# Kernel tuning notes

Measured on AMD Instinct MI355X. Metric: run time of the kernel, lower is better.

## Reference

```python
import math
import jax, jax.numpy as jnp
import numpy as np

N = 1600; C_IN = 16; HID = 64; OUT = 64; D_K = 8; N_HEADS = 8
CUTS = 8; NUM_RBF = 8; RBF_PROJ = 4; RADIUS = 6.0; ALPHA = 3.0

def leaky(x):
    return jnp.where(x >= 0, x, 0.2 * x)

def group_norm(x, gamma, beta, groups=4, eps=1e-5):
    # x: [N, C]; torch GroupNorm applied on [1, C, N]: stats over (C/groups, N) per group
    n, c = x.shape
    xg = x.T.reshape(groups, -1)
    mu = jnp.mean(xg, axis=1, keepdims=True)
    var = jnp.mean((xg - mu) ** 2, axis=1, keepdims=True)
    xn = ((xg - mu) * jax.lax.rsqrt(var + eps)).reshape(c, n).T
    return xn * gamma + beta

def setup_inputs():
    key = jax.random.key(0)
    ks = jax.random.split(key, 32)
    def rn(k, shape, s=0.1):
        return (jax.random.normal(k, shape) * s).astype(jnp.float32)
    return {
        "points": jax.random.normal(ks[0], (N, 3), jnp.float32),
        "nuv": jax.random.normal(ks[1], (N, 3, 3), jnp.float32),
        "features": jax.random.normal(ks[2], (N, C_IN), jnp.float32),
        "w_in1": rn(ks[3], (HID, C_IN)), "b_in1": rn(ks[4], (HID,)),
        "w_in2": rn(ks[5], (HID, HID)), "b_in2": rn(ks[6], (HID,)),
        "g_in": 1.0 + rn(ks[7], (HID,)), "be_in": rn(ks[8], (HID,)),
        "wq": rn(ks[9], (HID, HID)), "bq": rn(ks[10], (HID,)),
        "wk": rn(ks[11], (HID, HID)), "bk": rn(ks[12], (HID,)),
        "wv": rn(ks[13], (HID, HID)), "bv": rn(ks[14], (HID,)),
        "conv_w1": rn(ks[15], (CUTS, 4 + RBF_PROJ), 0.5),
        "conv_b1": jnp.abs(rn(ks[16], (CUTS,), 0.5)),
        "conv_w2": rn(ks[17], (HID, CUTS), 0.3), "conv_b2": rn(ks[18], (HID,), 0.3),
        "rbf_log_sigma": jnp.log(jnp.asarray(0.6 * 2.0 / (NUM_RBF - 1), jnp.float32)),
        "rbf_a": rn(ks[19], (RBF_PROJ, NUM_RBF), 0.3), "rbf_b": rn(ks[20], (RBF_PROJ,), 0.1),
        "rbf_centers": jnp.linspace(0.0, 2.0, NUM_RBF, dtype=jnp.float32),
        "w_o1": rn(ks[21], (OUT, HID)), "b_o1": rn(ks[22], (OUT,)),
        "w_o2": rn(ks[23], (OUT, OUT)), "b_o2": rn(ks[24], (OUT,)),
        "g_out": 1.0 + rn(ks[25], (OUT,)), "be_out": rn(ks[26], (OUT,)),
        "w_res": rn(ks[27], (OUT, C_IN)), "b_res": rn(ks[28], (OUT,)),
    }

def reference(points, nuv, features, w_in1, b_in1, w_in2, b_in2, g_in, be_in,
              wq, bq, wk, bk, wv, bv, conv_w1, conv_b1, conv_w2, conv_b2,
              rbf_log_sigma, rbf_a, rbf_b, rbf_centers,
              w_o1, b_o1, w_o2, b_o2, g_out, be_out, w_res, b_res):
    # point-wise MLP + GroupNorm
    h = leaky(features @ w_in1.T + b_in1)
    h = leaky(h @ w_in2.T + b_in2)
    h = group_norm(h, g_in, be_in)
    Q = h @ wq.T + bq
    K = h @ wk.T + bk
    V = h @ wv.T + bv
    pts = points / (math.sqrt(2.0) * RADIUS)
    diff = pts[None, :, :] - pts[:, None, :]            # [N, N, 3] = x_j - x_i
    n_i = nuv[:, 0, :]
    n_j = jax.lax.stop_gradient(n_i)                    # j-side normals are detached in the original
    ndot = jnp.einsum("ia,ja->ij", n_i, n_j)            # <n_i, n_j>
    d2 = jnp.sum(diff ** 2, axis=-1) * (2.0 - ndot) ** 2  # pseudo-geodesic squared distance
    W = (1.0 + d2 / ALPHA) ** (-ALPHA)                  # geodesic window weight
    d2_safe = jnp.where(d2 > 0, d2, 1.0)
    base_d = jnp.where(d2 > 0, jnp.sqrt(d2_safe), 0.0)  # safe sqrt (finite grad at 0)
    sigma = jnp.maximum(jnp.exp(rbf_log_sigma), 1e-6)
    R = jnp.exp(-((base_d[:, :, None] - rbf_centers) ** 2) / (2.0 * sigma ** 2))  # [N,N,NUM_RBF]
    R_proj = R @ rbf_a.T + rbf_b                        # [N, N, RBF_PROJ]
    X_loc = jnp.einsum("iab,ijb->ija", nuv, diff)       # local tangent-frame coords [N,N,3]
    X = jnp.concatenate([X_loc, ndot[:, :, None], R_proj], axis=-1)  # [N, N, 4+RBF_PROJ]
    F1 = jax.nn.relu(X @ conv_w1.T + conv_b1)           # shared conv layer-1 [N, N, CUTS]
    scale = 1.0 / math.sqrt(D_K)
    heads = []
    for h_id in range(N_HEADS):
        s = slice(h_id * D_K, (h_id + 1) * D_K)
        Fh = jax.nn.relu(F1 @ conv_w2[s].T + conv_b2[s])      # per-head conv weights [N, N, D_K]
        S = (Q[:, s] @ K[:, s].T) * scale                     # attention logits [N, N]
        P = jax.nn.softmax(S, axis=1) * W                     # softmax over j, fused with window
        heads.append(jnp.einsum("ij,ijc,jc->ic", P, Fh, V[:, s]))
    agg = jnp.concatenate(heads, axis=1)                      # [N, HID]
    o = leaky(agg @ w_o1.T + b_o1)
    o = leaky(o @ w_o2.T + b_o2)
    o = group_norm(o, g_out, be_out)
    return o + features @ w_res.T + b_res
```

## Files before the change

kernel.cpp:

```cpp
#include <hip/hip_runtime.h>

typedef __fp16 h2 __attribute__((ext_vector_type(2)));
typedef unsigned int u32;

#define NPTS 1600
#define NCHUNK 10
#define CHUNKJ 160
#define TILE 32
#define QS (0.35355339059327373f*1.4426950408889634f)
#define PSCALE 0.11785113019775793f
#define LOG2E 1.4426950408889634f

__device__ __forceinline__ float leaky(float x){ return x >= 0.f ? x : 0.2f*x; }
__device__ __forceinline__ float d4(float4 a, float4 b){ return a.x*b.x + a.y*b.y + a.z*b.z + a.w*b.w; }
__device__ __forceinline__ u32 pkn(float a, float b){ h2 v; v[0]=(__fp16)a; v[1]=(__fp16)b; return __builtin_bit_cast(u32,v); }
__device__ __forceinline__ h2 u2h(u32 u){ return __builtin_bit_cast(h2,u); }
__device__ __forceinline__ float dot2(h2 a, h2 b, float c){ return __builtin_amdgcn_fdot2(a,b,c,false); }
__device__ __forceinline__ u32 rfl(u32 x){ return (u32)__builtin_amdgcn_readfirstlane((int)x); }

__global__ __launch_bounds__(256) void k_in(
    const float* __restrict__ feat, const float* __restrict__ w1, const float* __restrict__ b1,
    const float* __restrict__ w2, const float* __restrict__ b2,
    const float* __restrict__ conv_w1, const float* __restrict__ conv_b1,
    const float* __restrict__ conv_w2,
    const float* __restrict__ rbf_a, const float* __restrict__ rbf_b,
    const float* __restrict__ rbf_ls, const float* __restrict__ rbf_c,
    float* __restrict__ h2out, float* __restrict__ bstat1, float* __restrict__ wpk)
{
  __shared__ float sh[4][64];
  __shared__ float sred[4][8];
  int t = threadIdx.x, w = t>>6, c = t&63;
  int i = blockIdx.x*4 + w;

  if (blockIdx.x == 0) {
    u32* wp = (u32*)wpk;
    {
      int row = t>>2, q = t&3;
      wp[32 + row*4 + q] = pkn(conv_w2[row*8+2*q], conv_w2[row*8+2*q+1]);
    }
    if (t < 32) {
      int cc = t>>2, kq = t&3;
      float a0=0.f, a1=0.f;
      #pragma unroll
      for (int p=0;p<4;p++){ a0 += conv_w1[cc*8+4+p]*rbf_a[p*8+2*kq]; a1 += conv_w1[cc*8+4+p]*rbf_a[p*8+2*kq+1]; }
      wp[cc*4+kq] = pkn(a0,a1);
    } else if (t < 40) {
      int cc = t-32; float s = conv_b1[cc];
      #pragma unroll
      for (int p=0;p<4;p++) s += conv_w1[cc*8+4+p]*rbf_b[p];
      wpk[288+cc] = s;
    } else if (t == 40) {
      float sig = fmaxf(expf(rbf_ls[0]), 1e-6f);
      float m = -LOG2E/(2.f*sig*sig);
      float c0 = rbf_c[0];
      float dl = rbf_c[1] - rbf_c[0];
      wpk[296] = c0;
      wpk[297] = m;
      wpk[298] = -2.f*m*dl;
      wpk[299] = m*dl*dl;
    }
  }

  const float4* f4 = (const float4*)(feat + i*16);
  float4 f0=f4[0], f1v=f4[1], f2v=f4[2], f3v=f4[3];
  const float4* w1r = (const float4*)(w1 + c*16);
  float h1 = b1[c] + d4(f0,w1r[0]) + d4(f1v,w1r[1]) + d4(f2v,w1r[2]) + d4(f3v,w1r[3]);
  h1 = leaky(h1);
  sh[w][c] = h1;
  __syncthreads();
  float hh = b2[c];
  #pragma unroll
  for (int k4=0;k4<16;k4++){
    float4 hv = *(const float4*)&sh[w][k4*4];
    hh += d4(hv, *(const float4*)&w2[c*64 + k4*4]);
  }
  hh = leaky(hh);
  h2out[i*64+c] = hh;

  float s = hh, qq = hh*hh;
  s += __shfl_xor(s,1);  qq += __shfl_xor(qq,1);
  s += __shfl_xor(s,2);  qq += __shfl_xor(qq,2);
  s += __shfl_xor(s,4);  qq += __shfl_xor(qq,4);
  s += __shfl_xor(s,8);  qq += __shfl_xor(qq,8);
  if ((c&15)==0){ int g=c>>4; sred[w][g]=s; sred[w][4+g]=qq; }
  __syncthreads();
  if (t<8) bstat1[blockIdx.x*8+t] = sred[0][t]+sred[1][t]+sred[2][t]+sred[3][t];
}

__global__ __launch_bounds__(256) void k_qkv(
  const float* __restrict__ h2b, const float* __restrict__ bstat1,
  const float* __restrict__ g_in, const float* __restrict__ be_in,
  const float* __restrict__ wq, const float* __restrict__ bq,
  const float* __restrict__ wk, const float* __restrict__ bk,
  const float* __restrict__ wv, const float* __restrict__ bv,
  float* __restrict__ Q, float* __restrict__ K, float* __restrict__ V)
{
  __shared__ float sh[4][64];
  __shared__ float sp[64];
  __shared__ float sst[8];
  int t=threadIdx.x, w=t>>6, c=t&63;
  int i = blockIdx.x*4 + w;
  if (t<64){ int g=t&7; float s=0.f;
    for (int m=t>>3; m<400; m+=8) s += bstat1[m*8+g];
    sp[t]=s; }
  __syncthreads();
  if (t<8){ float s=0.f;
    #pragma unroll
    for (int q=0;q<8;q++) s += sp[q*8+t];
    sst[t]=s; }
  __syncthreads();
  int g = c>>4;
  const float inv = 1.f/25600.f;
  float mu = sst[g]*inv;
  float var = sst[4+g]*inv - mu*mu;
  float rs = rsqrtf(var + 1e-5f);
  float hn = (h2b[i*64+c]-mu)*rs*g_in[c] + be_in[c];
  sh[w][c] = hn;
  __syncthreads();
  float q=bq[c], k=bk[c], v=bv[c];
  #pragma unroll
  for (int k4=0;k4<16;k4++){
    float4 hv = *(const float4*)&sh[w][k4*4];
    q += d4(hv, *(const float4*)&wq[c*64+k4*4]);
    k += d4(hv, *(const float4*)&wk[c*64+k4*4]);
    v += d4(hv, *(const float4*)&wv[c*64+k4*4]);
  }
  Q[i*64+c] = q*QS;
  K[i*64+c] = k;
  V[i*64+c] = v;
}

__global__ __launch_bounds__(256,4) void k_pair(
  const float* __restrict__ Qm, const float* __restrict__ Km, const float* __restrict__ Vm,
  const float* __restrict__ pts, const float* __restrict__ nuv,
  const float* __restrict__ w1, const float* __restrict__ wpk,
  const float* __restrict__ b2g, float* __restrict__ part)
{
  __shared__ __align__(16) float SM[4928];
  float* sQ  = SM;
  float* sK  = SM + 1088;
  u32*   sVp = (u32*)(SM + 3264);
  u32*   sWX = (u32*)(SM + 4352);
  float* sPt = SM + 4672;
  float* sNj = SM + 4800;
  float* sRed = SM;

  int t = threadIdx.x;
  int r = t & 15, jl = t >> 4;
  int bx = blockIdx.x;
  int rb = bx % 100, jc = bx / 100;
  int I0 = rb*16, J0 = jc*CHUNKJ;
  int i = I0 + r;

  { int row = t>>4, col = (t&15)<<2;
    *(float4*)&sQ[row*68+col] = *(const float4*)&Qm[(I0+row)*64 + col]; }
  if (t < 128) {
    int r2 = t>>3, cc = t&7, ib = (I0+r2)*9;
    float a0=w1[cc*8], a1=w1[cc*8+1], a2=w1[cc*8+2];
    float x = a0*nuv[ib+0] + a1*nuv[ib+3] + a2*nuv[ib+6];
    float y = a0*nuv[ib+1] + a1*nuv[ib+4] + a2*nuv[ib+7];
    float z = a0*nuv[ib+2] + a1*nuv[ib+5] + a2*nuv[ib+8];
    sWX[r2*20+cc*2+0] = pkn(x,y);
    sWX[r2*20+cc*2+1] = pkn(z, w1[cc*8+3]);
  }
  __syncthreads();
  u32 wxp[16];
  #pragma unroll
  for (int q2=0;q2<4;q2++) *(uint4*)&wxp[q2*4] = *(const uint4*)&sWX[r*20+q2*4];

  const u32* wp = (const u32*)wpk;
  h2 wr[8][4];
  #pragma unroll
  for (int cc=0;cc<8;cc++)
    #pragma unroll
    for (int q2=0;q2<4;q2++) wr[cc][q2] = u2h(rfl(wp[cc*4+q2]));
  const u32* w2p = wp + 32;
  const float* b1p = wpk + 288;
  float c0  = wpk[296];
  float mco = wpk[297];
  float C2  = wpk[298];
  float A1  = wpk[299];

  float pix = pts[i*3+0]*PSCALE, piy = pts[i*3+1]*PSCALE, piz = pts[i*3+2]*PSCALE;
  float nix = nuv[i*9+0], niy = nuv[i*9+1], niz = nuv[i*9+2];

  float acc[64];
  #pragma unroll
  for (int o=0;o<64;o++) acc[o] = 0.f;
  float lh[8];
  #pragma unroll
  for (int h=0;h<8;h++) lh[h] = 0.f;

  #pragma unroll 1
  for (int tb=0; tb<CHUNKJ; tb+=TILE) {
    int jbase = J0 + tb;
    __syncthreads();
    #pragma unroll
    for (int q2=0;q2<2;q2++) {
      int idx = t + q2*256;
      int row = idx >> 4, col = (idx & 15) << 2;
      *(float4*)&sK[row*68+col] = *(const float4*)&Km[(jbase+row)*64+col];
    }
    { int row = t>>4, col = (t&15)<<2;
      float4 a = *(const float4*)&Vm[(jbase+row)*64+col];
      float4 b = *(const float4*)&Vm[(jbase+16+row)*64+col];
      uint4 p; p.x=pkn(a.x,b.x); p.y=pkn(a.y,b.y); p.z=pkn(a.z,b.z); p.w=pkn(a.w,b.w);
      *(uint4*)&sVp[row*68+col] = p;
    }
    if (t < TILE) {
      int j = jbase + t;
      sPt[t*4+0]=pts[j*3+0]*PSCALE; sPt[t*4+1]=pts[j*3+1]*PSCALE; sPt[t*4+2]=pts[j*3+2]*PSCALE;
      sNj[t*4+0]=nuv[j*9+0]; sNj[t*4+1]=nuv[j*9+1]; sNj[t*4+2]=nuv[j*9+2];
    }
    __syncthreads();

    h2 F1p[2][4];
    float Wv[2];
    #pragma unroll
    for (int jj=0;jj<2;jj++) {
      int jloc = jl + (jj<<4);
      float dx = sPt[jloc*4+0]-pix, dy = sPt[jloc*4+1]-piy, dz = sPt[jloc*4+2]-piz;
      float ndot = nix*sNj[jloc*4+0] + niy*sNj[jloc*4+1] + niz*sNj[jloc*4+2];
      float d2r = dx*dx + dy*dy + dz*dz;
      float wf = 2.f - ndot;
      float d2 = d2r*wf*wf;
      float tp = fmaf(d2, 0.3333333333333333f, 1.f);
      Wv[jj] = __builtin_amdgcn_rcpf(tp*tp*tp);
      float dd = __builtin_amdgcn_sqrtf(d2);
      float g0 = dd - c0;
      float s2 = mco*g0*g0;
      float uu = C2*g0;
      float R[8];
      #pragma unroll
      for (int k=0;k<8;k++){
        float kf = (float)k, k2f = (float)(k*k);
        R[k] = __builtin_amdgcn_exp2f(fmaf(kf, uu, fmaf(k2f, A1, s2)));
      }
      h2 xv0; xv0[0]=(__fp16)dx; xv0[1]=(__fp16)dy;
      h2 xv1; xv1[0]=(__fp16)dz; xv1[1]=(__fp16)ndot;
      h2 r01=__builtin_amdgcn_cvt_pkrtz(R[0],R[1]);
      h2 r23=__builtin_amdgcn_cvt_pkrtz(R[2],R[3]);
      h2 r45=__builtin_amdgcn_cvt_pkrtz(R[4],R[5]);
      h2 r67=__builtin_amdgcn_cvt_pkrtz(R[6],R[7]);
      float F1f[8];
      #pragma unroll
      for (int cc=0;cc<8;cc++){
        float f = dot2(r67, wr[cc][3], b1p[cc]);
        f = dot2(r45, wr[cc][2], f);
        f = dot2(r23, wr[cc][1], f);
        f = dot2(r01, wr[cc][0], f);
        f = dot2(u2h(wxp[cc*2+1]), xv1, f);
        f = dot2(u2h(wxp[cc*2+0]), xv0, f);
        F1f[cc] = fmaxf(f, 0.f);
      }
      F1p[jj][0]=__builtin_amdgcn_cvt_pkrtz(F1f[0],F1f[1]);
      F1p[jj][1]=__builtin_amdgcn_cvt_pkrtz(F1f[2],F1f[3]);
      F1p[jj][2]=__builtin_amdgcn_cvt_pkrtz(F1f[4],F1f[5]);
      F1p[jj][3]=__builtin_amdgcn_cvt_pkrtz(F1f[6],F1f[7]);
    }

    #pragma unroll
    for (int h=0;h<8;h++) {
      float4 q0 = *(const float4*)&sQ[r*68+h*8];
      float4 q1 = *(const float4*)&sQ[r*68+h*8+4];
      float4 ka0 = *(const float4*)&sK[jl*68+h*8];
      float4 ka1 = *(const float4*)&sK[jl*68+h*8+4];
      float4 kb0 = *(const float4*)&sK[(jl+16)*68+h*8];
      float4 kb1 = *(const float4*)&sK[(jl+16)*68+h*8+4];
      float S0 = d4(q0,ka0) + d4(q1,ka1);
      float S1 = d4(q0,kb0) + d4(q1,kb1);
      float e0 = __builtin_amdgcn_exp2f(S0);
      float e1 = __builtin_amdgcn_exp2f(S1);
      lh[h] += e0 + e1;
      h2 ewp; ewp[0]=(__fp16)(e0*Wv[0]); ewp[1]=(__fp16)(e1*Wv[1]);
      uint4 vpA = *(const uint4*)&sVp[jl*68+h*8];
      uint4 vpB = *(const uint4*)&sVp[jl*68+h*8+4];
      u32 vparr[8] = {vpA.x,vpA.y,vpA.z,vpA.w,vpB.x,vpB.y,vpB.z,vpB.w};
      #pragma unroll
      for (int cc=0;cc<8;cc++){
        int rw = h*8+cc;
        h2 w0=u2h(w2p[rw*4+0]), w1h=u2h(w2p[rw*4+1]), w2h=u2h(w2p[rw*4+2]), w3h=u2h(w2p[rw*4+3]);
        float b2v = b2g[rw];
        float fh0 = dot2(F1p[0][0],w0, dot2(F1p[0][1],w1h, dot2(F1p[0][2],w2h, dot2(F1p[0][3],w3h, b2v))));
        float fh1 = dot2(F1p[1][0],w0, dot2(F1p[1][1],w1h, dot2(F1p[1][2],w2h, dot2(F1p[1][3],w3h, b2v))));
        h2 fhp = __builtin_amdgcn_cvt_pkrtz(fmaxf(fh0,0.f), fmaxf(fh1,0.f));
        h2 ev = u2h(vparr[cc]) * ewp;
        acc[rw] = dot2(fhp, ev, acc[rw]);
      }
    }
  }

  #pragma unroll
  for (int o=0;o<64;o++){ acc[o] += __shfl_xor(acc[o],16); acc[o] += __shfl_xor(acc[o],32); }
  #pragma unroll
  for (int h=0;h<8;h++){ lh[h] += __shfl_xor(lh[h],16); lh[h] += __shfl_xor(lh[h],32); }
  __syncthreads();
  int wv = t >> 6, lane = t & 63;
  if (lane < 16) {
    #pragma unroll
    for (int o=0;o<64;o++) sRed[(wv*16+lane)*72+o] = acc[o];
    #pragma unroll
    for (int h=0;h<8;h++) sRed[(wv*16+lane)*72+64+h] = lh[h];
  }
  __syncthreads();
  for (int v2 = t; v2 < 16*72; v2 += 256) {
    int rr = v2/72, o = v2 - rr*72;
    part[(jc*NPTS + I0 + rr)*72 + o] =
      sRed[(0*16+rr)*72+o] + sRed[(1*16+rr)*72+o] + sRed[(2*16+rr)*72+o] + sRed[(3*16+rr)*72+o];
  }
}

__global__ __launch_bounds__(256) void k_agg(
  const float* __restrict__ part, const float* __restrict__ w_o1, const float* __restrict__ b_o1,
  const float* __restrict__ w_o2, const float* __restrict__ b_o2,
  float* __restrict__ o2b, float* __restrict__ bstat2)
{
  __shared__ float sh[4][64];
  __shared__ float sred[4][8];
  int t = threadIdx.x, w = t>>6, c = t&63;
  int i = blockIdx.x*4 + w;
  int h = c>>3;
  float a = 0.f, L = 0.f;
  #pragma unroll
  for (int jc=0;jc<NCHUNK;jc++){
    const float* p = part + (jc*NPTS + i)*72;
    a += p[c]; L += p[64+h];
  }
  float agg = a / L;
  sh[w][c] = agg; __syncthreads();
  float o1 = b_o1[c];
  #pragma unroll
  for (int k4=0;k4<16;k4++){
    float4 hv = *(const float4*)&sh[w][k4*4];
    o1 += d4(hv, *(const float4*)&w_o1[c*64+k4*4]);
  }
  o1 = leaky(o1);
  __syncthreads();
  sh[w][c] = o1; __syncthreads();
  float o2 = b_o2[c];
  #pragma unroll
  for (int k4=0;k4<16;k4++){
    float4 hv = *(const float4*)&sh[w][k4*4];
    o2 += d4(hv, *(const float4*)&w_o2[c*64+k4*4]);
  }
  o2 = leaky(o2);
  o2b[i*64+c] = o2;

  float s = o2, qq = o2*o2;
  s += __shfl_xor(s,1);  qq += __shfl_xor(qq,1);
  s += __shfl_xor(s,2);  qq += __shfl_xor(qq,2);
  s += __shfl_xor(s,4);  qq += __shfl_xor(qq,4);
  s += __shfl_xor(s,8);  qq += __shfl_xor(qq,8);
  if ((c&15)==0){ int g=c>>4; sred[w][g]=s; sred[w][4+g]=qq; }
  __syncthreads();
  if (t<8) bstat2[blockIdx.x*8+t] = sred[0][t]+sred[1][t]+sred[2][t]+sred[3][t];
}

__global__ __launch_bounds__(256) void k_out(
  const float* __restrict__ o2b, const float* __restrict__ bstat2,
  const float* __restrict__ g_out, const float* __restrict__ be_out,
  const float* __restrict__ feat, const float* __restrict__ w_res, const float* __restrict__ b_res,
  float* __restrict__ out)
{
  __shared__ float sp[64];
  __shared__ float sst[8];
  int t = threadIdx.x, w = t>>6, c = t&63;
  int i = blockIdx.x*4 + w;
  if (t<64){ int g=t&7; float s=0.f;
    for (int m=t>>3; m<400; m+=8) s += bstat2[m*8+g];
    sp[t]=s; }
  __syncthreads();
  if (t<8){ float s=0.f;
    #pragma unroll
    for (int q=0;q<8;q++) s += sp[q*8+t];
    sst[t]=s; }
  __syncthreads();
  int g = c>>4;
  const float inv = 1.f/25600.f;
  float mu = sst[g]*inv;
  float var = sst[4+g]*inv - mu*mu;
  float rs = rsqrtf(var + 1e-5f);
  float on = (o2b[i*64+c]-mu)*rs*g_out[c] + be_out[c];
  const float4* f4 = (const float4*)(feat + i*16);
  const float4* wr = (const float4*)(w_res + c*16);
  float res = b_res[c] + d4(f4[0],wr[0]) + d4(f4[1],wr[1]) + d4(f4[2],wr[2]) + d4(f4[3],wr[3]);
  out[i*64+c] = on + res;
}

extern "C" void kernel_launch(void* const* d_in, const int* in_sizes, int n_in,
                              void* d_out, int out_size, void* d_ws, size_t ws_size,
                              hipStream_t stream) {
  const float* points  = (const float*)d_in[0];
  const float* nuv     = (const float*)d_in[1];
  const float* feat    = (const float*)d_in[2];
  const float* w_in1   = (const float*)d_in[3];
  const float* b_in1   = (const float*)d_in[4];
  const float* w_in2   = (const float*)d_in[5];
  const float* b_in2   = (const float*)d_in[6];
  const float* g_in    = (const float*)d_in[7];
  const float* be_in   = (const float*)d_in[8];
  const float* wq      = (const float*)d_in[9];
  const float* bq      = (const float*)d_in[10];
  const float* wk      = (const float*)d_in[11];
  const float* bk      = (const float*)d_in[12];
  const float* wv      = (const float*)d_in[13];
  const float* bv      = (const float*)d_in[14];
  const float* conv_w1 = (const float*)d_in[15];
  const float* conv_b1 = (const float*)d_in[16];
  const float* conv_w2 = (const float*)d_in[17];
  const float* conv_b2 = (const float*)d_in[18];
  const float* rbf_ls  = (const float*)d_in[19];
  const float* rbf_a   = (const float*)d_in[20];
  const float* rbf_b   = (const float*)d_in[21];
  const float* rbf_c   = (const float*)d_in[22];
  const float* w_o1    = (const float*)d_in[23];
  const float* b_o1    = (const float*)d_in[24];
  const float* w_o2    = (const float*)d_in[25];
  const float* b_o2    = (const float*)d_in[26];
  const float* g_out   = (const float*)d_in[27];
  const float* be_out  = (const float*)d_in[28];
  const float* w_res   = (const float*)d_in[29];
  const float* b_res   = (const float*)d_in[30];

  float* ws     = (float*)d_ws;
  float* h2f    = ws;
  float* Qb     = ws + 102400;
  float* Kb     = ws + 204800;
  float* Vb     = ws + 307200;
  float* bstat1 = ws + 409600;
  float* bstat2 = ws + 412800;
  float* wpk    = ws + 416000;
  float* part   = ws + 416320;
  float* o2b    = ws + 1568320;
  float* out    = (float*)d_out;

  k_in<<<400, 256, 0, stream>>>(feat, w_in1, b_in1, w_in2, b_in2,
                                conv_w1, conv_b1, conv_w2, rbf_a, rbf_b, rbf_ls, rbf_c,
                                h2f, bstat1, wpk);
  k_qkv<<<400, 256, 0, stream>>>(h2f, bstat1, g_in, be_in, wq, bq, wk, bk, wv, bv, Qb, Kb, Vb);
  k_pair<<<1000, 256, 0, stream>>>(Qb, Kb, Vb, points, nuv, conv_w1, wpk, conv_b2, part);
  k_agg<<<400, 256, 0, stream>>>(part, w_o1, b_o1, w_o2, b_o2, o2b, bstat2);
  k_out<<<400, 256, 0, stream>>>(o2b, bstat2, g_out, be_out, feat, w_res, b_res, out);
}
```

Before: 270.1 us.

## Fuse input/QKV and agg/output kernels using software grid barriers

Merges k_in with k_qkv, and k_agg with k_out, into two kernels that sync through an atomic-counter grid barrier, so the group-norm statistics are reduced across blocks without a separate launch. The h2 and o2 intermediates stay in registers and are no longer written to and re-read from global memory. The counters are reset with a memset each call, and k_pair's launch_bounds occupancy hint is removed. This relies on all 400 blocks being co-resident, since otherwise the barrier would deadlock, and it adds a memset launch.

```diff
diff --git a/kernel.cpp b/kernel.cpp
--- a/kernel.cpp
+++ b/kernel.cpp
@@ -18,17 +18,35 @@
 __device__ __forceinline__ float dot2(h2 a, h2 b, float c){ return __builtin_amdgcn_fdot2(a,b,c,false); }
 __device__ __forceinline__ u32 rfl(u32 x){ return (u32)__builtin_amdgcn_readfirstlane((int)x); }
 
-__global__ __launch_bounds__(256) void k_in(
+__device__ __forceinline__ void gbar(u32* ctr, u32 target){
+  __threadfence();
+  __syncthreads();
+  if (threadIdx.x == 0){
+    atomicAdd(ctr, 1u);
+    while (__hip_atomic_load(ctr, __ATOMIC_ACQUIRE, __HIP_MEMORY_SCOPE_AGENT) < target)
+      __builtin_amdgcn_s_sleep(2);
+  }
+  __syncthreads();
+}
+
+__global__ __launch_bounds__(256) void k_h(
     const float* __restrict__ feat, const float* __restrict__ w1, const float* __restrict__ b1,
     const float* __restrict__ w2, const float* __restrict__ b2,
     const float* __restrict__ conv_w1, const float* __restrict__ conv_b1,
     const float* __restrict__ conv_w2,
     const float* __restrict__ rbf_a, const float* __restrict__ rbf_b,
     const float* __restrict__ rbf_ls, const float* __restrict__ rbf_c,
-    float* __restrict__ h2out, float* __restrict__ bstat1, float* __restrict__ wpk)
+    const float* __restrict__ g_in, const float* __restrict__ be_in,
+    const float* __restrict__ wq, const float* __restrict__ bq,
+    const float* __restrict__ wk, const float* __restrict__ bk,
+    const float* __restrict__ wv, const float* __restrict__ bv,
+    float* __restrict__ Q, float* __restrict__ K, float* __restrict__ V,
+    float* __restrict__ bstat1, float* __restrict__ wpk, u32* __restrict__ ctr)
 {
   __shared__ float sh[4][64];
   __shared__ float sred[4][8];
+  __shared__ float sp[64];
+  __shared__ float sst[8];
   int t = threadIdx.x, w = t>>6, c = t&63;
   int i = blockIdx.x*4 + w;
 
@@ -75,7 +93,6 @@
     hh += d4(hv, *(const float4*)&w2[c*64 + k4*4]);
   }
   hh = leaky(hh);
-  h2out[i*64+c] = hh;
 
   float s = hh, qq = hh*hh;
   s += __shfl_xor(s,1);  qq += __shfl_xor(qq,1);
@@ -85,36 +102,26 @@
   if ((c&15)==0){ int g=c>>4; sred[w][g]=s; sred[w][4+g]=qq; }
   __syncthreads();
   if (t<8) bstat1[blockIdx.x*8+t] = sred[0][t]+sred[1][t]+sred[2][t]+sred[3][t];
-}
-
-__global__ __launch_bounds__(256) void k_qkv(
-  const float* __restrict__ h2b, const float* __restrict__ bstat1,
-  const float* __restrict__ g_in, const float* __restrict__ be_in,
-  const float* __restrict__ wq, const float* __restrict__ bq,
-  const float* __restrict__ wk, const float* __restrict__ bk,
-  const float* __restrict__ wv, const float* __restrict__ bv,
-  float* __restrict__ Q, float* __restrict__ K, float* __restrict__ V)
-{
-  __shared__ float sh[4][64];
-  __shared__ float sp[64];
-  __shared__ float sst[8];
-  int t=threadIdx.x, w=t>>6, c=t&63;
-  int i = blockIdx.x*4 + w;
-  if (t<64){ int g=t&7; float s=0.f;
-    for (int m=t>>3; m<400; m+=8) s += bstat1[m*8+g];
-    sp[t]=s; }
-  __syncthreads();
-  if (t<8){ float s=0.f;
-    #pragma unroll
-    for (int q=0;q<8;q++) s += sp[q*8+t];
-    sst[t]=s; }
+
+  gbar(ctr, 400u);
+
+  if (t<64){ int g=t&7; float sacc=0.f;
+    for (int m=t>>3; m<400; m+=8)
+      sacc += __hip_atomic_load(&bstat1[m*8+g], __ATOMIC_RELAXED, __HIP_MEMORY_SCOPE_AGENT);
+    sp[t]=sacc; }
+  __syncthreads();
+  if (t<8){ float sacc=0.f;
+    #pragma unroll
+    for (int q=0;q<8;q++) sacc += sp[q*8+t];
+    sst[t]=sacc; }
   __syncthreads();
   int g = c>>4;
   const float inv = 1.f/25600.f;
   float mu = sst[g]*inv;
   float var = sst[4+g]*inv - mu*mu;
   float rs = rsqrtf(var + 1e-5f);
-  float hn = (h2b[i*64+c]-mu)*rs*g_in[c] + be_in[c];
+  float hn = (hh-mu)*rs*g_in[c] + be_in[c];
+  __syncthreads();
   sh[w][c] = hn;
   __syncthreads();
   float q=bq[c], k=bk[c], v=bv[c];
@@ -130,7 +137,7 @@
   V[i*64+c] = v;
 }
 
-__global__ __launch_bounds__(256,4) void k_pair(
+__global__ __launch_bounds__(256) void k_pair(
   const float* __restrict__ Qm, const float* __restrict__ Km, const float* __restrict__ Vm,
   const float* __restrict__ pts, const float* __restrict__ nuv,
   const float* __restrict__ w1, const float* __restrict__ wpk,
@@ -310,13 +317,17 @@
   }
 }
 
-__global__ __launch_bounds__(256) void k_agg(
+__global__ __launch_bounds__(256) void k_tail(
   const float* __restrict__ part, const float* __restrict__ w_o1, const float* __restrict__ b_o1,
   const float* __restrict__ w_o2, const float* __restrict__ b_o2,
-  float* __restrict__ o2b, float* __restrict__ bstat2)
+  const float* __restrict__ g_out, const float* __restrict__ be_out,
+  const float* __restrict__ feat, const float* __restrict__ w_res, const float* __restrict__ b_res,
+  float* __restrict__ bstat2, u32* __restrict__ ctr, float* __restrict__ out)
 {
   __shared__ float sh[4][64];
   __shared__ float sred[4][8];
+  __shared__ float sp[64];
+  __shared__ float sst[8];
   int t = threadIdx.x, w = t>>6, c = t&63;
   int i = blockIdx.x*4 + w;
   int h = c>>3;
@@ -344,7 +355,6 @@
     o2 += d4(hv, *(const float4*)&w_o2[c*64+k4*4]);
   }
   o2 = leaky(o2);
-  o2b[i*64+c] = o2;
 
   float s = o2, qq = o2*o2;
   s += __shfl_xor(s,1);  qq += __shfl_xor(qq,1);
@@ -354,36 +364,28 @@
   if ((c&15)==0){ int g=c>>4; sred[w][g]=s; sred[w][4+g]=qq; }
   __syncthreads();
   if (t<8) bstat2[blockIdx.x*8+t] = sred[0][t]+sred[1][t]+sred[2][t]+sred[3][t];
-}
-
-__global__ __launch_bounds__(256) void k_out(
-  const float* __restrict__ o2b, const float* __restrict__ bstat2,
-  const float* __restrict__ g_out, const float* __restrict__ be_out,
-  const float* __restrict__ feat, const float* __restrict__ w_res, const float* __restrict__ b_res,
-  float* __restrict__ out)
-{
-  __shared__ float sp[64];
-  __shared__ float sst[8];
-  int t = threadIdx.x, w = t>>6, c = t&63;
-  int i = blockIdx.x*4 + w;
-  if (t<64){ int g=t&7; float s=0.f;
-    for (int m=t>>3; m<400; m+=8) s += bstat2[m*8+g];
-    sp[t]=s; }
-  __syncthreads();
-  if (t<8){ float s=0.f;
-    #pragma unroll
-    for (int q=0;q<8;q++) s += sp[q*8+t];
-    sst[t]=s; }
+
+  gbar(ctr, 400u);
+
+  if (t<64){ int g=t&7; float sacc=0.f;
+    for (int m=t>>3; m<400; m+=8)
+      sacc += __hip_atomic_load(&bstat2[m*8+g], __ATOMIC_RELAXED, __HIP_MEMORY_SCOPE_AGENT);
+    sp[t]=sacc; }
+  __syncthreads();
+  if (t<8){ float sacc=0.f;
+    #pragma unroll
+    for (int q=0;q<8;q++) sacc += sp[q*8+t];
+    sst[t]=sacc; }
   __syncthreads();
   int g = c>>4;
   const float inv = 1.f/25600.f;
   float mu = sst[g]*inv;
   float var = sst[4+g]*inv - mu*mu;
   float rs = rsqrtf(var + 1e-5f);
-  float on = (o2b[i*64+c]-mu)*rs*g_out[c] + be_out[c];
+  float on = (o2-mu)*rs*g_out[c] + be_out[c];
   const float4* f4 = (const float4*)(feat + i*16);
-  const float4* wr = (const float4*)(w_res + c*16);
-  float res = b_res[c] + d4(f4[0],wr[0]) + d4(f4[1],wr[1]) + d4(f4[2],wr[2]) + d4(f4[3],wr[3]);
+  const float4* wrr = (const float4*)(w_res + c*16);
+  float res = b_res[c] + d4(f4[0],wrr[0]) + d4(f4[1],wrr[1]) + d4(f4[2],wrr[2]) + d4(f4[3],wrr[3]);
   out[i*64+c] = on + res;
 }
 
@@ -423,22 +425,22 @@
   const float* b_res   = (const float*)d_in[30];
 
   float* ws     = (float*)d_ws;
-  float* h2f    = ws;
-  float* Qb     = ws + 102400;
-  float* Kb     = ws + 204800;
-  float* Vb     = ws + 307200;
-  float* bstat1 = ws + 409600;
-  float* bstat2 = ws + 412800;
-  float* wpk    = ws + 416000;
-  float* part   = ws + 416320;
-  float* o2b    = ws + 1568320;
+  float* Qb     = ws;
+  float* Kb     = ws + 102400;
+  float* Vb     = ws + 204800;
+  float* bstat1 = ws + 307200;
+  float* bstat2 = ws + 310400;
+  float* wpk    = ws + 313600;
+  u32*   ctr    = (u32*)(ws + 313920);
+  float* part   = ws + 313924;
   float* out    = (float*)d_out;
 
-  k_in<<<400, 256, 0, stream>>>(feat, w_in1, b_in1, w_in2, b_in2,
-                                conv_w1, conv_b1, conv_w2, rbf_a, rbf_b, rbf_ls, rbf_c,
-                                h2f, bstat1, wpk);
-  k_qkv<<<400, 256, 0, stream>>>(h2f, bstat1, g_in, be_in, wq, bq, wk, bk, wv, bv, Qb, Kb, Vb);
+  hipMemsetAsync(ctr, 0, 16, stream);
+  k_h<<<400, 256, 0, stream>>>(feat, w_in1, b_in1, w_in2, b_in2,
+                               conv_w1, conv_b1, conv_w2, rbf_a, rbf_b, rbf_ls, rbf_c,
+                               g_in, be_in, wq, bq, wk, bk, wv, bv,
+                               Qb, Kb, Vb, bstat1, wpk, ctr);
   k_pair<<<1000, 256, 0, stream>>>(Qb, Kb, Vb, points, nuv, conv_w1, wpk, conv_b2, part);
-  k_agg<<<400, 256, 0, stream>>>(part, w_o1, b_o1, w_o2, b_o2, o2b, bstat2);
-  k_out<<<400, 256, 0, stream>>>(o2b, bstat2, g_out, be_out, feat, w_res, b_res, out);
+  k_tail<<<400, 256, 0, stream>>>(part, w_o1, b_o1, w_o2, b_o2, g_out, be_out,
+                                  feat, w_res, b_res, bstat2, ctr+1, out);
 }
```

Measured after the change: 344.3 us. 1.27x slower.
